# Performance work log

Measured on AMD Instinct MI355X. Metric: run time of the kernel, lower is better.

Reference implementation:

```python
import jax, jax.numpy as jnp
import numpy as np

B, T = 64, 1000
Q_DIM, M_DIM, A_DIM = 1024, 512, 128
N_FILT, KSIZE = 32, 31
PAD = (KSIZE - 1) // 2


def setup_inputs() -> dict:
    key = jax.random.key(0)
    ks = jax.random.split(key, 12)
    inp = {
        "query": jax.random.normal(ks[0], (B, Q_DIM), dtype=jnp.float32),
        "memory": jax.random.normal(ks[1], (B, T, M_DIM), dtype=jnp.float32),
        "attention_weights_cum": jax.random.uniform(ks[2], (B, 1, T), dtype=jnp.float32),
        "mask": jnp.zeros((B, T), dtype=bool),
        # params (Linear weights stored [out, in] like torch)
        "Wq": jax.random.normal(ks[3], (A_DIM, Q_DIM), dtype=jnp.float32) * 0.03,
        "bq": jnp.zeros((A_DIM,), dtype=jnp.float32),
        "Wm": jax.random.normal(ks[4], (A_DIM, M_DIM), dtype=jnp.float32) * 0.04,
        "bm": jnp.zeros((A_DIM,), dtype=jnp.float32),
        "Wv": jax.random.normal(ks[5], (1, A_DIM), dtype=jnp.float32) * 0.09,
        "bv": jnp.zeros((1,), dtype=jnp.float32),
        "conv_w": jax.random.normal(ks[6], (N_FILT, 1, KSIZE), dtype=jnp.float32) * 0.18,
        "conv_b": jnp.zeros((N_FILT,), dtype=jnp.float32),
        "Wloc": jax.random.normal(ks[7], (A_DIM, N_FILT), dtype=jnp.float32) * 0.18,
    }
    return inp


def reference(query, memory, attention_weights_cum, mask,
              Wq, bq, Wm, bm, Wv, bv, conv_w, conv_b, Wloc):
    # key projection: [B, T, A]
    key = jnp.einsum('btm,am->bta', memory, Wm) + bm
    # query projection: [B, 1, A]
    q = (query @ Wq.T + bq)[:, None, :]
    # location conv: [B,1,T] -> [B,N_FILT,T]
    loc = jax.lax.conv_general_dilated(
        attention_weights_cum, conv_w, window_strides=(1,),
        padding=[(PAD, PAD)], dimension_numbers=('NCH', 'OIH', 'NCH'))
    loc = loc + conv_b[None, :, None]
    # [B, T, A]
    loc = jnp.einsum('bft,af->bta', loc, Wloc)
    # energies: [B, T]
    energies = (jnp.tanh(q + loc + key) @ Wv.T + bv)[..., 0]
    alignment = jnp.where(mask, -jnp.inf, energies)
    attention_weights = jax.nn.softmax(alignment, axis=1)  # [B, T]
    attention_context = jnp.einsum('bt,btm->bm', attention_weights, memory)
    return attention_context, attention_weights
```

## Files before the change

kernel.cpp:

```cpp
#include <hip/hip_runtime.h>
#include <math.h>

#define Bsz 64
#define Tn 1000
#define QD 1024
#define MD 512
#define AD 128
#define NF 32
#define KS 31
#define PADc 15

#define TTB 32
#define AS_ROW 520

typedef __attribute__((ext_vector_type(8))) short bf16x8;
typedef __attribute__((ext_vector_type(4))) float f32x4;

static __device__ __forceinline__ short f2bf(float x) {
    unsigned u = __float_as_uint(x);
    unsigned r = (u + 0x7fffu + ((u >> 16) & 1u)) >> 16;
    return (short)r;
}

static __device__ __forceinline__ float fast_tanh(float x) {
    float e2 = __expf(2.f * x);
    return 1.f - 2.f / (e2 + 1.f);
}

__global__ __launch_bounds__(256)
void k_prep(const float* __restrict__ Wm, const float* __restrict__ conv_w,
            const float* __restrict__ conv_b, const float* __restrict__ Wloc,
            const float* __restrict__ query, const float* __restrict__ Wq,
            const float* __restrict__ bq, const float* __restrict__ bm,
            short* __restrict__ WmF, short* __restrict__ W2F,
            float* __restrict__ qsum) {
    __shared__ float qs[QD];
    __shared__ float red[256];
    int bid = blockIdx.x;
    if (bid < 32) {
        int g = bid * 256 + threadIdx.x;
        int wc = g >> 6, l = g & 63;
        int a = (wc >> 4) * 16 + (l & 15);
        int kb = (wc & 15) * 32 + (l >> 4) * 8;
        const float* src = Wm + a * MD + kb;
        float4 v0 = *(const float4*)src;
        float4 v1 = *(const float4*)(src + 4);
        bf16x8 o;
        o[0] = f2bf(v0.x); o[1] = f2bf(v0.y); o[2] = f2bf(v0.z); o[3] = f2bf(v0.w);
        o[4] = f2bf(v1.x); o[5] = f2bf(v1.y); o[6] = f2bf(v1.z); o[7] = f2bf(v1.w);
        *(bf16x8*)(WmF + (size_t)g * 8) = o;
    } else if (bid < 96) {
        int b = bid - 32;
        int a = threadIdx.x & 127;
        int half = threadIdx.x >> 7;
        for (int i = threadIdx.x; i < QD; i += 256) qs[i] = query[b * QD + i];
        __syncthreads();
        const float4* Wq4 = (const float4*)(Wq + a * QD + half * (QD / 2));
        const float4* qs4 = (const float4*)(qs + half * (QD / 2));
        float acc = 0.f;
#pragma unroll 4
        for (int i = 0; i < QD / 8; ++i) {
            float4 w = Wq4[i];
            float4 q = qs4[i];
            acc += w.x * q.x + w.y * q.y + w.z * q.z + w.w * q.w;
        }
        red[threadIdx.x] = acc;
        __syncthreads();
        if (half == 0) {
            float b2 = 0.f;
            for (int f = 0; f < NF; ++f) b2 += conv_b[f] * Wloc[a * NF + f];
            qsum[b * AD + a] = red[a] + red[a + 128] + bq[a] + bm[a] + b2;
        }
    } else {
        for (int s = threadIdx.x * 2; s < threadIdx.x * 2 + 2; ++s) {
            int w = s >> 6, l = s & 63;
            int a = w * 16 + (l & 15);
            int kb = (l >> 4) * 8;
            bf16x8 o;
#pragma unroll
            for (int j = 0; j < 8; ++j) {
                int k = kb + j;
                float sum = 0.f;
                if (k < KS)
                    for (int f = 0; f < NF; ++f) sum += conv_w[f * KS + k] * Wloc[a * NF + f];
                o[j] = f2bf(sum);
            }
            *(bf16x8*)(W2F + s * 8) = o;
        }
    }
}

__global__ __launch_bounds__(512)
void k_energies(const float* __restrict__ mem, const float* __restrict__ awc,
                const short* __restrict__ WmF, const short* __restrict__ W2F,
                const float* __restrict__ Wv, const float* __restrict__ bv,
                const float* __restrict__ qsum, float* __restrict__ energies) {
    __shared__ short As[TTB * AS_ROW];
    __shared__ float ered[8][TTB + 1];

    int b = blockIdx.y;
    int t0 = blockIdx.x * TTB;
    int tid = threadIdx.x;
    int w = tid >> 6;
    int lane = tid & 63;
    int m16 = lane & 15;
    int q = lane >> 4;

    bf16x8 bf[17];
    const bf16x8* bp = (const bf16x8*)WmF;
#pragma unroll
    for (int c = 0; c < 16; ++c) bf[c] = bp[(w * 16 + c) * 64 + lane];
    bf[16] = ((const bf16x8*)W2F)[w * 64 + lane];

    const float* base = mem + ((size_t)b * Tn + t0) * MD;
#pragma unroll
    for (int r = 0; r < 8; ++r) {
        int i = tid + r * 512;
        int t = i >> 7;
        int k = (i & 127) * 4;
        float4 v = make_float4(0.f, 0.f, 0.f, 0.f);
        if (t0 + t < Tn) v = *(const float4*)(base + t * MD + k);
        short4 o;
        o.x = f2bf(v.x); o.y = f2bf(v.y); o.z = f2bf(v.z); o.w = f2bf(v.w);
        *(short4*)&As[t * AS_ROW + k] = o;
    }
    __syncthreads();

    f32x4 acc0 = {0.f, 0.f, 0.f, 0.f}, acc1 = acc0;
#pragma unroll
    for (int c = 0; c < 16; ++c) {
        bf16x8 a0 = *(const bf16x8*)&As[m16 * AS_ROW + c * 32 + q * 8];
        bf16x8 a1 = *(const bf16x8*)&As[(16 + m16) * AS_ROW + c * 32 + q * 8];
        acc0 = __builtin_amdgcn_mfma_f32_16x16x32_bf16(a0, bf[c], acc0, 0, 0, 0);
        acc1 = __builtin_amdgcn_mfma_f32_16x16x32_bf16(a1, bf[c], acc1, 0, 0, 0);
    }
    {
        bf16x8 a0, a1;
        int tA = t0 + m16, tB = tA + 16;
#pragma unroll
        for (int j = 0; j < 8; ++j) {
            int kk = q * 8 + j;
            int s0 = tA + kk - PADc, s1 = tB + kk - PADc;
            float v0 = (kk < KS && s0 >= 0 && s0 < Tn) ? awc[b * Tn + s0] : 0.f;
            float v1 = (kk < KS && s1 >= 0 && s1 < Tn) ? awc[b * Tn + s1] : 0.f;
            a0[j] = f2bf(v0);
            a1[j] = f2bf(v1);
        }
        acc0 = __builtin_amdgcn_mfma_f32_16x16x32_bf16(a0, bf[16], acc0, 0, 0, 0);
        acc1 = __builtin_amdgcn_mfma_f32_16x16x32_bf16(a1, bf[16], acc1, 0, 0, 0);
    }

    int a = w * 16 + m16;
    float wvv = Wv[a];
    float qsv = qsum[b * AD + a];
#pragma unroll
    for (int r = 0; r < 4; ++r) {
        float e0 = wvv * fast_tanh(acc0[r] + qsv);
        float e1 = wvv * fast_tanh(acc1[r] + qsv);
#pragma unroll
        for (int m2 = 1; m2 < 16; m2 <<= 1) {
            e0 += __shfl_xor(e0, m2, 64);
            e1 += __shfl_xor(e1, m2, 64);
        }
        if (m16 == 0) {
            ered[w][q * 4 + r] = e0;
            ered[w][16 + q * 4 + r] = e1;
        }
    }
    __syncthreads();
    if (tid < TTB) {
        float E = bv[0];
#pragma unroll
        for (int ww = 0; ww < 8; ++ww) E += ered[ww][tid];
        int t = t0 + tid;
        if (t < Tn) energies[b * Tn + t] = E;
    }
}

__global__ __launch_bounds__(256)
void k_softmax(const float* __restrict__ energies, const unsigned char* __restrict__ mask,
               float* __restrict__ wout, float* __restrict__ ctx) {
    int b = blockIdx.x;
    int tid = threadIdx.x;
    __shared__ float red[256];

    ctx[b * MD + tid] = 0.f;
    ctx[b * MD + 256 + tid] = 0.f;

    float e[4];
    float lmax = -1e30f;
#pragma unroll
    for (int i = 0; i < 4; ++i) {
        int t = tid + i * 256;
        float v = -1e30f;
        if (t < Tn) {
            v = energies[b * Tn + t];
            if (mask[b * Tn + t]) v = -1e30f;
        }
        e[i] = v;
        lmax = fmaxf(lmax, v);
    }
    red[tid] = lmax;
    __syncthreads();
    for (int s = 128; s > 0; s >>= 1) {
        if (tid < s) red[tid] = fmaxf(red[tid], red[tid + s]);
        __syncthreads();
    }
    float smax = red[0];
    __syncthreads();

    float ex[4];
    float lsum = 0.f;
#pragma unroll
    for (int i = 0; i < 4; ++i) {
        ex[i] = __expf(e[i] - smax);
        lsum += ex[i];
    }
    red[tid] = lsum;
    __syncthreads();
    for (int s = 128; s > 0; s >>= 1) {
        if (tid < s) red[tid] += red[tid + s];
        __syncthreads();
    }
    float inv = 1.f / red[0];
#pragma unroll
    for (int i = 0; i < 4; ++i) {
        int t = tid + i * 256;
        if (t < Tn) wout[b * Tn + t] = ex[i] * inv;
    }
}

__global__ __launch_bounds__(256)
void k_context(const float* __restrict__ mem, const float* __restrict__ w,
               float* __restrict__ ctx) {
    int tc = blockIdx.x;
    int b = blockIdx.y;
    int tid = threadIdx.x;
    __shared__ float ws[64];
    int tstart = tc * 64;
    if (tid < 64) {
        int tt = tstart + tid;
        ws[tid] = (tt < Tn) ? w[b * Tn + tt] : 0.f;
    }
    __syncthreads();
    const float* mb = mem + (size_t)b * Tn * MD + tid * 2;
    float a0 = 0.f, a1 = 0.f;
    int nrow = (tstart + 64 <= Tn) ? 64 : (Tn - tstart);
    for (int i = 0; i < nrow; ++i) {
        float wv = ws[i];
        float2 v = *(const float2*)(mb + (size_t)(tstart + i) * MD);
        a0 += wv * v.x;
        a1 += wv * v.y;
    }
    atomicAdd(&ctx[b * MD + tid * 2], a0);
    atomicAdd(&ctx[b * MD + tid * 2 + 1], a1);
}

extern "C" void kernel_launch(void* const* d_in, const int* in_sizes, int n_in,
                              void* d_out, int out_size, void* d_ws, size_t ws_size,
                              hipStream_t stream) {
    const float* query  = (const float*)d_in[0];
    const float* memory = (const float*)d_in[1];
    const float* awc    = (const float*)d_in[2];
    const unsigned char* mask = (const unsigned char*)d_in[3];
    const float* Wq     = (const float*)d_in[4];
    const float* bq     = (const float*)d_in[5];
    const float* Wm     = (const float*)d_in[6];
    const float* bm     = (const float*)d_in[7];
    const float* Wv     = (const float*)d_in[8];
    const float* bv     = (const float*)d_in[9];
    const float* conv_w = (const float*)d_in[10];
    const float* conv_b = (const float*)d_in[11];
    const float* Wloc   = (const float*)d_in[12];

    float* out = (float*)d_out;
    float* ctx = out;
    float* wout = out + Bsz * MD;

    float* ws = (float*)d_ws;
    float* qsum  = ws;
    float* energ = ws + 8192;
    short* WmF = (short*)((char*)d_ws + 288768);
    short* W2F = (short*)((char*)d_ws + 288768 + 131072);

    k_prep<<<dim3(97), dim3(256), 0, stream>>>(Wm, conv_w, conv_b, Wloc, query, Wq,
                                               bq, bm, WmF, W2F, qsum);
    k_energies<<<dim3((Tn + TTB - 1) / TTB, Bsz), dim3(512), 0, stream>>>(
        memory, awc, WmF, W2F, Wv, bv, qsum, energ);
    k_softmax<<<dim3(Bsz), dim3(256), 0, stream>>>(energ, mask, wout, ctx);
    k_context<<<dim3(16, Bsz), dim3(256), 0, stream>>>(memory, wout, ctx);
}
```

Before: 296.9 us.

## Pre-convert memory to bf16 in workspace and swizzle the energies LDS tile

```diff
diff --git a/kernel.cpp b/kernel.cpp
--- a/kernel.cpp
+++ b/kernel.cpp
@@ -11,10 +11,13 @@
 #define PADc 15
 
 #define TTB 32
-#define AS_ROW 520
 
 typedef __attribute__((ext_vector_type(8))) short bf16x8;
 typedef __attribute__((ext_vector_type(4))) float f32x4;
+
+#define MEMB_OFF 428032
+#define MEMB_BYTES 65536000
+#define WS_NEED (MEMB_OFF + MEMB_BYTES)
 
 static __device__ __forceinline__ short f2bf(float x) {
     unsigned u = __float_as_uint(x);
@@ -25,6 +28,23 @@
 static __device__ __forceinline__ float fast_tanh(float x) {
     float e2 = __expf(2.f * x);
     return 1.f - 2.f / (e2 + 1.f);
+}
+
+__global__ __launch_bounds__(256)
+void k_convert(const float* __restrict__ mem, short* __restrict__ memB) {
+    int g = blockIdx.x * 256 + threadIdx.x;
+#pragma unroll
+    for (int u = 0; u < 8; ++u) {
+        size_t e = (size_t)(g + u * 524288) * 8;
+        if (e < (size_t)Bsz * Tn * MD) {
+            float4 v0 = *(const float4*)(mem + e);
+            float4 v1 = *(const float4*)(mem + e + 4);
+            bf16x8 o;
+            o[0] = f2bf(v0.x); o[1] = f2bf(v0.y); o[2] = f2bf(v0.z); o[3] = f2bf(v0.w);
+            o[4] = f2bf(v1.x); o[5] = f2bf(v1.y); o[6] = f2bf(v1.z); o[7] = f2bf(v1.w);
+            *(bf16x8*)(memB + e) = o;
+        }
+    }
 }
 
 __global__ __launch_bounds__(256)
@@ -90,13 +110,14 @@
     }
 }
 
+template <bool USE_BF16>
 __global__ __launch_bounds__(512)
-void k_energies(const float* __restrict__ mem, const float* __restrict__ awc,
+void k_energies(const float* __restrict__ mem, const short* __restrict__ memB,
+                const float* __restrict__ awc,
                 const short* __restrict__ WmF, const short* __restrict__ W2F,
                 const float* __restrict__ Wv, const float* __restrict__ bv,
                 const float* __restrict__ qsum, float* __restrict__ energies) {
-    __shared__ short As[TTB * AS_ROW];
-    __shared__ float ered[8][TTB + 1];
+    __shared__ short As[TTB * 64 * 8];
 
     int b = blockIdx.y;
     int t0 = blockIdx.x * TTB;
@@ -112,25 +133,35 @@
     for (int c = 0; c < 16; ++c) bf[c] = bp[(w * 16 + c) * 64 + lane];
     bf[16] = ((const bf16x8*)W2F)[w * 64 + lane];
 
-    const float* base = mem + ((size_t)b * Tn + t0) * MD;
-#pragma unroll
-    for (int r = 0; r < 8; ++r) {
-        int i = tid + r * 512;
-        int t = i >> 7;
-        int k = (i & 127) * 4;
-        float4 v = make_float4(0.f, 0.f, 0.f, 0.f);
-        if (t0 + t < Tn) v = *(const float4*)(base + t * MD + k);
-        short4 o;
-        o.x = f2bf(v.x); o.y = f2bf(v.y); o.z = f2bf(v.z); o.w = f2bf(v.w);
-        *(short4*)&As[t * AS_ROW + k] = o;
+#pragma unroll
+    for (int u = 0; u < 4; ++u) {
+        int g = tid + u * 512;
+        int row = g >> 6;
+        int col = g & 63;
+        int t = t0 + row;
+        bf16x8 v = {0, 0, 0, 0, 0, 0, 0, 0};
+        if (t < Tn) {
+            if (USE_BF16) {
+                v = *(const bf16x8*)(memB + (((size_t)b * Tn + t) << 9) + col * 8);
+            } else {
+                const float* src = mem + ((size_t)b * Tn + t) * MD + col * 8;
+                float4 v0 = *(const float4*)src;
+                float4 v1 = *(const float4*)(src + 4);
+                v[0] = f2bf(v0.x); v[1] = f2bf(v0.y); v[2] = f2bf(v0.z); v[3] = f2bf(v0.w);
+                v[4] = f2bf(v1.x); v[5] = f2bf(v1.y); v[6] = f2bf(v1.z); v[7] = f2bf(v1.w);
+            }
+        }
+        *(bf16x8*)&As[((row << 6) | (col ^ (row & 7))) * 8] = v;
     }
     __syncthreads();
 
     f32x4 acc0 = {0.f, 0.f, 0.f, 0.f}, acc1 = acc0;
+    int x0 = m16 & 7, r1 = 16 + m16;
 #pragma unroll
     for (int c = 0; c < 16; ++c) {
-        bf16x8 a0 = *(const bf16x8*)&As[m16 * AS_ROW + c * 32 + q * 8];
-        bf16x8 a1 = *(const bf16x8*)&As[(16 + m16) * AS_ROW + c * 32 + q * 8];
+        int u = c * 4 + q;
+        bf16x8 a0 = *(const bf16x8*)&As[((m16 << 6) | (u ^ x0)) * 8];
+        bf16x8 a1 = *(const bf16x8*)&As[((r1 << 6) | (u ^ x0)) * 8];
         acc0 = __builtin_amdgcn_mfma_f32_16x16x32_bf16(a0, bf[c], acc0, 0, 0, 0);
         acc1 = __builtin_amdgcn_mfma_f32_16x16x32_bf16(a1, bf[c], acc1, 0, 0, 0);
     }
@@ -150,6 +181,8 @@
         acc1 = __builtin_amdgcn_mfma_f32_16x16x32_bf16(a1, bf[16], acc1, 0, 0, 0);
     }
 
+    __syncthreads();
+    float* ered = (float*)As;
     int a = w * 16 + m16;
     float wvv = Wv[a];
     float qsv = qsum[b * AD + a];
@@ -163,15 +196,15 @@
             e1 += __shfl_xor(e1, m2, 64);
         }
         if (m16 == 0) {
-            ered[w][q * 4 + r] = e0;
-            ered[w][16 + q * 4 + r] = e1;
+            ered[w * 33 + q * 4 + r] = e0;
+            ered[w * 33 + 16 + q * 4 + r] = e1;
         }
     }
     __syncthreads();
     if (tid < TTB) {
         float E = bv[0];
 #pragma unroll
-        for (int ww = 0; ww < 8; ++ww) E += ered[ww][tid];
+        for (int ww = 0; ww < 8; ++ww) E += ered[ww * 33 + tid];
         int t = t0 + tid;
         if (t < Tn) energies[b * Tn + t] = E;
     }
@@ -282,11 +315,20 @@
     float* energ = ws + 8192;
     short* WmF = (short*)((char*)d_ws + 288768);
     short* W2F = (short*)((char*)d_ws + 288768 + 131072);
+    short* memB = (short*)((char*)d_ws + MEMB_OFF);
+
+    bool use_bf16 = (ws_size >= (size_t)WS_NEED);
 
     k_prep<<<dim3(97), dim3(256), 0, stream>>>(Wm, conv_w, conv_b, Wloc, query, Wq,
                                                bq, bm, WmF, W2F, qsum);
-    k_energies<<<dim3((Tn + TTB - 1) / TTB, Bsz), dim3(512), 0, stream>>>(
-        memory, awc, WmF, W2F, Wv, bv, qsum, energ);
+    if (use_bf16) {
+        k_convert<<<dim3(2048), dim3(256), 0, stream>>>(memory, memB);
+        k_energies<true><<<dim3((Tn + TTB - 1) / TTB, Bsz), dim3(512), 0, stream>>>(
+            memory, memB, awc, WmF, W2F, Wv, bv, qsum, energ);
+    } else {
+        k_energies<false><<<dim3((Tn + TTB - 1) / TTB, Bsz), dim3(512), 0, stream>>>(
+            memory, memB, awc, WmF, W2F, Wv, bv, qsum, energ);
+    }
     k_softmax<<<dim3(Bsz), dim3(256), 0, stream>>>(energ, mask, wout, ctx);
     k_context<<<dim3(16, Bsz), dim3(256), 0, stream>>>(memory, wout, ctx);
 }
```

After: 310.9 us. 4.7% more time.

## Fuse energies, online softmax and context into one flash-style kernel

Applied to the files above, without the earlier changes.

```diff
diff --git a/kernel.cpp b/kernel.cpp
--- a/kernel.cpp
+++ b/kernel.cpp
@@ -10,8 +10,9 @@
 #define KS 31
 #define PADc 15
 
-#define TTB 32
-#define AS_ROW 520
+#define NCH 16
+#define RPC 64
+#define SUB 16
 
 typedef __attribute__((ext_vector_type(8))) short bf16x8;
 typedef __attribute__((ext_vector_type(4))) float f32x4;
@@ -21,7 +22,9 @@
     unsigned r = (u + 0x7fffu + ((u >> 16) & 1u)) >> 16;
     return (short)r;
 }
-
+static __device__ __forceinline__ float bf2f(short s) {
+    return __uint_as_float(((unsigned)(unsigned short)s) << 16);
+}
 static __device__ __forceinline__ float fast_tanh(float x) {
     float e2 = __expf(2.f * x);
     return 1.f - 2.f / (e2 + 1.f);
@@ -91,15 +94,19 @@
 }
 
 __global__ __launch_bounds__(512)
-void k_energies(const float* __restrict__ mem, const float* __restrict__ awc,
-                const short* __restrict__ WmF, const short* __restrict__ W2F,
-                const float* __restrict__ Wv, const float* __restrict__ bv,
-                const float* __restrict__ qsum, float* __restrict__ energies) {
-    __shared__ short As[TTB * AS_ROW];
-    __shared__ float ered[8][TTB + 1];
+void k_fused(const float* __restrict__ mem, const float* __restrict__ awc,
+             const unsigned char* __restrict__ mask,
+             const short* __restrict__ WmF, const short* __restrict__ W2F,
+             const float* __restrict__ Wv, const float* __restrict__ bv,
+             const float* __restrict__ qsum, float* __restrict__ energ,
+             float* __restrict__ ctxc, float2* __restrict__ ml) {
+    __shared__ short As[2][SUB * 64 * 8];
+    __shared__ float ered[8][SUB + 1];
+    __shared__ float es[SUB], ps[SUB];
 
     int b = blockIdx.y;
-    int t0 = blockIdx.x * TTB;
+    int c = blockIdx.x;
+    int t0 = c * RPC;
     int tid = threadIdx.x;
     int w = tid >> 6;
     int lane = tid & 63;
@@ -109,151 +116,162 @@
     bf16x8 bf[17];
     const bf16x8* bp = (const bf16x8*)WmF;
 #pragma unroll
-    for (int c = 0; c < 16; ++c) bf[c] = bp[(w * 16 + c) * 64 + lane];
+    for (int cc = 0; cc < 16; ++cc) bf[cc] = bp[(w * 16 + cc) * 64 + lane];
     bf[16] = ((const bf16x8*)W2F)[w * 64 + lane];
-
-    const float* base = mem + ((size_t)b * Tn + t0) * MD;
-#pragma unroll
-    for (int r = 0; r < 8; ++r) {
-        int i = tid + r * 512;
-        int t = i >> 7;
-        int k = (i & 127) * 4;
-        float4 v = make_float4(0.f, 0.f, 0.f, 0.f);
-        if (t0 + t < Tn) v = *(const float4*)(base + t * MD + k);
-        short4 o;
-        o.x = f2bf(v.x); o.y = f2bf(v.y); o.z = f2bf(v.z); o.w = f2bf(v.w);
-        *(short4*)&As[t * AS_ROW + k] = o;
-    }
-    __syncthreads();
-
-    f32x4 acc0 = {0.f, 0.f, 0.f, 0.f}, acc1 = acc0;
-#pragma unroll
-    for (int c = 0; c < 16; ++c) {
-        bf16x8 a0 = *(const bf16x8*)&As[m16 * AS_ROW + c * 32 + q * 8];
-        bf16x8 a1 = *(const bf16x8*)&As[(16 + m16) * AS_ROW + c * 32 + q * 8];
-        acc0 = __builtin_amdgcn_mfma_f32_16x16x32_bf16(a0, bf[c], acc0, 0, 0, 0);
-        acc1 = __builtin_amdgcn_mfma_f32_16x16x32_bf16(a1, bf[c], acc1, 0, 0, 0);
-    }
-    {
-        bf16x8 a0, a1;
-        int tA = t0 + m16, tB = tA + 16;
-#pragma unroll
-        for (int j = 0; j < 8; ++j) {
-            int kk = q * 8 + j;
-            int s0 = tA + kk - PADc, s1 = tB + kk - PADc;
-            float v0 = (kk < KS && s0 >= 0 && s0 < Tn) ? awc[b * Tn + s0] : 0.f;
-            float v1 = (kk < KS && s1 >= 0 && s1 < Tn) ? awc[b * Tn + s1] : 0.f;
-            a0[j] = f2bf(v0);
-            a1[j] = f2bf(v1);
-        }
-        acc0 = __builtin_amdgcn_mfma_f32_16x16x32_bf16(a0, bf[16], acc0, 0, 0, 0);
-        acc1 = __builtin_amdgcn_mfma_f32_16x16x32_bf16(a1, bf[16], acc1, 0, 0, 0);
-    }
 
     int a = w * 16 + m16;
     float wvv = Wv[a];
     float qsv = qsum[b * AD + a];
-#pragma unroll
-    for (int r = 0; r < 4; ++r) {
-        float e0 = wvv * fast_tanh(acc0[r] + qsv);
-        float e1 = wvv * fast_tanh(acc1[r] + qsv);
-#pragma unroll
-        for (int m2 = 1; m2 < 16; m2 <<= 1) {
-            e0 += __shfl_xor(e0, m2, 64);
-            e1 += __shfl_xor(e1, m2, 64);
-        }
-        if (m16 == 0) {
-            ered[w][q * 4 + r] = e0;
-            ered[w][16 + q * 4 + r] = e1;
-        }
+    float bv0 = bv[0];
+
+    float ctxj = 0.f;
+    float m_run = -1e30f, l_run = 0.f;
+
+    float4 vreg[4];
+
+    auto load_sub = [&](int s) {
+#pragma unroll
+        for (int i = 0; i < 2; ++i) {
+            int g = tid + i * 512;
+            int row = g >> 6;
+            int col = g & 63;
+            int t = t0 + s * SUB + row;
+            if (t < Tn) {
+                const float* src = mem + ((size_t)b * Tn + t) * MD + col * 8;
+                vreg[i * 2] = *(const float4*)src;
+                vreg[i * 2 + 1] = *(const float4*)(src + 4);
+            } else {
+                vreg[i * 2] = make_float4(0.f, 0.f, 0.f, 0.f);
+                vreg[i * 2 + 1] = vreg[i * 2];
+            }
+        }
+    };
+    auto write_sub = [&](int buf) {
+#pragma unroll
+        for (int i = 0; i < 2; ++i) {
+            int g = tid + i * 512;
+            int row = g >> 6;
+            int col = g & 63;
+            float4 v0 = vreg[i * 2], v1 = vreg[i * 2 + 1];
+            bf16x8 o;
+            o[0] = f2bf(v0.x); o[1] = f2bf(v0.y); o[2] = f2bf(v0.z); o[3] = f2bf(v0.w);
+            o[4] = f2bf(v1.x); o[5] = f2bf(v1.y); o[6] = f2bf(v1.z); o[7] = f2bf(v1.w);
+            *(bf16x8*)&As[buf][((row << 6) | (col ^ (row & 7))) * 8] = o;
+        }
+    };
+
+    load_sub(0);
+    write_sub(0);
+
+    for (int s = 0; s < 4; ++s) {
+        __syncthreads();
+        if (s < 3) load_sub(s + 1);
+
+        int buf = s & 1;
+        const short* tile = As[buf];
+
+        f32x4 acc = {0.f, 0.f, 0.f, 0.f};
+        int x0 = m16 & 7;
+#pragma unroll
+        for (int cc = 0; cc < 16; ++cc) {
+            int u = cc * 4 + q;
+            bf16x8 af = *(const bf16x8*)&tile[((m16 << 6) | (u ^ x0)) * 8];
+            acc = __builtin_amdgcn_mfma_f32_16x16x32_bf16(af, bf[cc], acc, 0, 0, 0);
+        }
+        {
+            int trow = t0 + s * SUB + m16;
+            bf16x8 af;
+#pragma unroll
+            for (int j = 0; j < 8; ++j) {
+                int kk = q * 8 + j;
+                int ts = trow + kk - PADc;
+                float v = (kk < KS && ts >= 0 && ts < Tn) ? awc[b * Tn + ts] : 0.f;
+                af[j] = f2bf(v);
+            }
+            acc = __builtin_amdgcn_mfma_f32_16x16x32_bf16(af, bf[16], acc, 0, 0, 0);
+        }
+
+#pragma unroll
+        for (int r = 0; r < 4; ++r) {
+            float e = wvv * fast_tanh(acc[r] + qsv);
+#pragma unroll
+            for (int m2 = 1; m2 < 16; m2 <<= 1) e += __shfl_xor(e, m2, 64);
+            if (m16 == 0) ered[w][q * 4 + r] = e;
+        }
+        __syncthreads();
+        if (tid < SUB) {
+            float E = bv0;
+#pragma unroll
+            for (int ww = 0; ww < 8; ++ww) E += ered[ww][tid];
+            int t = t0 + s * SUB + tid;
+            bool valid = (t < Tn);
+            bool msk = valid ? (mask[b * Tn + t] != 0) : true;
+            if (valid) energ[b * Tn + t] = E;
+            es[tid] = (valid && !msk) ? E : -1e30f;
+        }
+        __syncthreads();
+
+        float mx = m_run;
+#pragma unroll
+        for (int r = 0; r < SUB; ++r) mx = fmaxf(mx, es[r]);
+        if (tid < SUB) ps[tid] = (es[tid] <= -1e29f) ? 0.f : __expf(es[tid] - mx);
+        __syncthreads();
+        float alpha = __expf(m_run - mx);
+        float psum = 0.f, cacc = 0.f;
+#pragma unroll
+        for (int r = 0; r < SUB; ++r) {
+            float p = ps[r];
+            psum += p;
+            short sv = tile[((r << 6) | ((tid >> 3) ^ (r & 7))) * 8 + (tid & 7)];
+            cacc += p * bf2f(sv);
+        }
+        ctxj = ctxj * alpha + cacc;
+        l_run = l_run * alpha + psum;
+        m_run = mx;
+
+        if (s < 3) write_sub((s + 1) & 1);
+    }
+
+    ctxc[((size_t)c * Bsz + b) * MD + tid] = ctxj;
+    if (tid == 0) ml[c * Bsz + b] = make_float2(m_run, l_run);
+}
+
+__global__ __launch_bounds__(512)
+void k_combine(const float* __restrict__ ctxc, const float2* __restrict__ ml,
+               const float* __restrict__ energ, const unsigned char* __restrict__ mask,
+               float* __restrict__ ctx, float* __restrict__ wout) {
+    __shared__ float sm[NCH], sl[NCH];
+    int b = blockIdx.x;
+    int tid = threadIdx.x;
+    if (tid < NCH) {
+        float2 v = ml[tid * Bsz + b];
+        sm[tid] = v.x;
+        sl[tid] = v.y;
     }
     __syncthreads();
-    if (tid < TTB) {
-        float E = bv[0];
-#pragma unroll
-        for (int ww = 0; ww < 8; ++ww) E += ered[ww][tid];
-        int t = t0 + tid;
-        if (t < Tn) energies[b * Tn + t] = E;
+    float M = -1e30f;
+#pragma unroll
+    for (int cc = 0; cc < NCH; ++cc) M = fmaxf(M, sm[cc]);
+    float L = 0.f;
+#pragma unroll
+    for (int cc = 0; cc < NCH; ++cc) L += sl[cc] * __expf(sm[cc] - M);
+    float inv = 1.f / L;
+
+    float s = 0.f;
+#pragma unroll
+    for (int cc = 0; cc < NCH; ++cc)
+        s += ctxc[((size_t)cc * Bsz + b) * MD + tid] * __expf(sm[cc] - M);
+    ctx[b * MD + tid] = s * inv;
+
+#pragma unroll
+    for (int i = 0; i < 2; ++i) {
+        int t = tid + i * 512;
+        if (t < Tn) {
+            bool msk = mask[b * Tn + t] != 0;
+            float e = energ[b * Tn + t];
+            wout[b * Tn + t] = msk ? 0.f : __expf(e - M) * inv;
+        }
     }
-}
-
-__global__ __launch_bounds__(256)
-void k_softmax(const float* __restrict__ energies, const unsigned char* __restrict__ mask,
-               float* __restrict__ wout, float* __restrict__ ctx) {
-    int b = blockIdx.x;
-    int tid = threadIdx.x;
-    __shared__ float red[256];
-
-    ctx[b * MD + tid] = 0.f;
-    ctx[b * MD + 256 + tid] = 0.f;
-
-    float e[4];
-    float lmax = -1e30f;
-#pragma unroll
-    for (int i = 0; i < 4; ++i) {
-        int t = tid + i * 256;
-        float v = -1e30f;
-        if (t < Tn) {
-            v = energies[b * Tn + t];
-            if (mask[b * Tn + t]) v = -1e30f;
-        }
-        e[i] = v;
-        lmax = fmaxf(lmax, v);
-    }
-    red[tid] = lmax;
-    __syncthreads();
-    for (int s = 128; s > 0; s >>= 1) {
-        if (tid < s) red[tid] = fmaxf(red[tid], red[tid + s]);
-        __syncthreads();
-    }
-    float smax = red[0];
-    __syncthreads();
-
-    float ex[4];
-    float lsum = 0.f;
-#pragma unroll
-    for (int i = 0; i < 4; ++i) {
-        ex[i] = __expf(e[i] - smax);
-        lsum += ex[i];
-    }
-    red[tid] = lsum;
-    __syncthreads();
-    for (int s = 128; s > 0; s >>= 1) {
-        if (tid < s) red[tid] += red[tid + s];
-        __syncthreads();
-    }
-    float inv = 1.f / red[0];
-#pragma unroll
-    for (int i = 0; i < 4; ++i) {
-        int t = tid + i * 256;
-        if (t < Tn) wout[b * Tn + t] = ex[i] * inv;
-    }
-}
-
-__global__ __launch_bounds__(256)
-void k_context(const float* __restrict__ mem, const float* __restrict__ w,
-               float* __restrict__ ctx) {
-    int tc = blockIdx.x;
-    int b = blockIdx.y;
-    int tid = threadIdx.x;
-    __shared__ float ws[64];
-    int tstart = tc * 64;
-    if (tid < 64) {
-        int tt = tstart + tid;
-        ws[tid] = (tt < Tn) ? w[b * Tn + tt] : 0.f;
-    }
-    __syncthreads();
-    const float* mb = mem + (size_t)b * Tn * MD + tid * 2;
-    float a0 = 0.f, a1 = 0.f;
-    int nrow = (tstart + 64 <= Tn) ? 64 : (Tn - tstart);
-    for (int i = 0; i < nrow; ++i) {
-        float wv = ws[i];
-        float2 v = *(const float2*)(mb + (size_t)(tstart + i) * MD);
-        a0 += wv * v.x;
-        a1 += wv * v.y;
-    }
-    atomicAdd(&ctx[b * MD + tid * 2], a0);
-    atomicAdd(&ctx[b * MD + tid * 2 + 1], a1);
 }
 
 extern "C" void kernel_launch(void* const* d_in, const int* in_sizes, int n_in,
@@ -277,16 +295,16 @@
     float* ctx = out;
     float* wout = out + Bsz * MD;
 
-    float* ws = (float*)d_ws;
-    float* qsum  = ws;
-    float* energ = ws + 8192;
+    float* qsum  = (float*)d_ws;
+    float* energ = (float*)d_ws + 8192;
     short* WmF = (short*)((char*)d_ws + 288768);
     short* W2F = (short*)((char*)d_ws + 288768 + 131072);
+    float2* ml = (float2*)((char*)d_ws + 428032);
+    float* ctxc = (float*)((char*)d_ws + 436224);
 
     k_prep<<<dim3(97), dim3(256), 0, stream>>>(Wm, conv_w, conv_b, Wloc, query, Wq,
                                                bq, bm, WmF, W2F, qsum);
-    k_energies<<<dim3((Tn + TTB - 1) / TTB, Bsz), dim3(512), 0, stream>>>(
-        memory, awc, WmF, W2F, Wv, bv, qsum, energ);
-    k_softmax<<<dim3(Bsz), dim3(256), 0, stream>>>(energ, mask, wout, ctx);
-    k_context<<<dim3(16, Bsz), dim3(256), 0, stream>>>(memory, wout, ctx);
-}
+    k_fused<<<dim3(NCH, Bsz), dim3(512), 0, stream>>>(
+        memory, awc, mask, WmF, W2F, Wv, bv, qsum, energ, ctxc, ml);
+    k_combine<<<dim3(Bsz), dim3(512), 0, stream>>>(ctxc, ml, energ, mask, ctx, wout);
+}
```

New measurement: 309.2 us. +4.1%, slower.
